# Optimization experiments

Hardware: AMD Instinct MI355X
Metric: run time of the kernel (lower is better)

Reference implementation:

```python
import jax, jax.numpy as jnp
import numpy as np

B, D, A, H, NH = 32768, 768, 17, 128, 4
DH = H // NH


def _ln(x, g, b, eps=1e-5):
    mu = jnp.mean(x, axis=-1, keepdims=True)
    var = jnp.mean((x - mu) ** 2, axis=-1, keepdims=True)
    return (x - mu) / jnp.sqrt(var + eps) * g + b


def setup_inputs() -> dict:
    key = jax.random.key(0)
    ks = jax.random.split(key, 16)
    s = 0.02
    return {
        "visual_feat": jax.random.normal(ks[0], (B, D), jnp.float32),
        "au_feat": jax.random.uniform(ks[1], (B, A), jnp.float32),
        "w_tok": jax.random.normal(ks[2], (H, 1), jnp.float32) * s,
        "b_tok": jnp.zeros((H,), jnp.float32),
        "pos": jax.random.normal(ks[3], (1, A, H), jnp.float32) * s,
        "g_auln": jnp.ones((H,), jnp.float32),
        "b_auln": jnp.zeros((H,), jnp.float32),
        "w_q": jax.random.normal(ks[4], (H, D), jnp.float32) * s,
        "b_q": jnp.zeros((H,), jnp.float32),
        "w_in": jax.random.normal(ks[5], (3 * H, H), jnp.float32) * s,  # packed q,k,v in_proj
        "b_in": jnp.zeros((3 * H,), jnp.float32),
        "w_ao": jax.random.normal(ks[6], (H, H), jnp.float32) * s,  # MHA out_proj
        "b_ao": jnp.zeros((H,), jnp.float32),
        "g_aln": jnp.ones((H,), jnp.float32),
        "b_aln": jnp.zeros((H,), jnp.float32),
        "w_out": jax.random.normal(ks[7], (D, H), jnp.float32) * s,
        "b_out": jnp.zeros((D,), jnp.float32),
        "w_gate": jax.random.normal(ks[8], (D, 2 * D), jnp.float32) * s,
        "b_gate": jnp.zeros((D,), jnp.float32),
    }


def reference(visual_feat, au_feat, w_tok, b_tok, pos, g_auln, b_auln,
              w_q, b_q, w_in, b_in, w_ao, b_ao, g_aln, b_aln,
              w_out, b_out, w_gate, b_gate):
    # AU tokens: Linear(1 -> H) on intensities, + pos embed, LN. [B, A, H]
    au_tokens = au_feat[..., None] * w_tok[:, 0] + b_tok
    au_tokens = _ln(au_tokens + pos, g_auln, b_auln)
    # query: [B, H] (seq len 1)
    query = visual_feat @ w_q.T + b_q
    # MultiheadAttention (batch_first, packed in_proj)
    wq, wk, wv = w_in[:H], w_in[H:2 * H], w_in[2 * H:]
    bq, bk, bv = b_in[:H], b_in[H:2 * H], b_in[2 * H:]
    q = (query @ wq.T + bq).reshape(-1, NH, DH)          # [B, nh, dh]
    k = (au_tokens @ wk.T + bk).reshape(-1, A, NH, DH)   # [B, A, nh, dh]
    v = (au_tokens @ wv.T + bv).reshape(-1, A, NH, DH)
    scale = 1.0 / jnp.sqrt(jnp.asarray(DH, q.dtype))
    scores = jnp.einsum('bhd,bahd->bha', q * scale, k)   # [B, nh, A]
    attn = jax.nn.softmax(scores, axis=-1)
    ctx = jnp.einsum('bha,bahd->bhd', attn, v).reshape(-1, H)
    attn_out = ctx @ w_ao.T + b_ao
    attn_out = _ln(attn_out, g_aln, b_aln)
    attn_feat = attn_out @ w_out.T + b_out               # [B, D]
    gate_in = jnp.concatenate([visual_feat, attn_feat], axis=1)
    gate = jax.nn.sigmoid(gate_in @ w_gate.T + b_gate)
    return gate * attn_feat + (1.0 - gate) * visual_feat
```

## Files before the change

### kernel.cpp

```cpp
#include <hip/hip_runtime.h>
#include <hip/hip_bf16.h>

typedef __hip_bfloat16 bf16;
typedef __attribute__((ext_vector_type(8))) short short8;
typedef __attribute__((ext_vector_type(4))) float f32x4;
typedef __attribute__((ext_vector_type(8))) __bf16 bf16x8;

#define NB 32768
#define DD 768
#define AA 17
#define HH 128

__device__ __forceinline__ float bs2f(short s){
  unsigned int u = ((unsigned int)(unsigned short)s) << 16;
  return __builtin_bit_cast(float, u);
}
__device__ __forceinline__ short f2bs(float f){
  bf16 h = __float2bfloat16(f);
  return __builtin_bit_cast(short, h);
}
__device__ __forceinline__ f32x4 mfma16(short8 a, short8 b, f32x4 c){
  return __builtin_amdgcn_mfma_f32_16x16x32_bf16(
      __builtin_bit_cast(bf16x8, a), __builtin_bit_cast(bf16x8, b), c, 0, 0, 0);
}

template<int F32>
__device__ __forceinline__ short8 ldchunk(const void* base, long elem_off){
  if (F32){
    const float4* p = (const float4*)((const float*)base + elem_off);
    float4 x = p[0], y = p[1];
    short8 r;
    r[0]=f2bs(x.x); r[1]=f2bs(x.y); r[2]=f2bs(x.z); r[3]=f2bs(x.w);
    r[4]=f2bs(y.x); r[5]=f2bs(y.y); r[6]=f2bs(y.z); r[7]=f2bs(y.w);
    return r;
  } else {
    return *(const short8*)((const short*)base + elem_off);
  }
}


__device__ __forceinline__ float blk_mean128(float v, float* tmp){
  int t = threadIdx.x;
  #pragma unroll
  for (int m = 32; m; m >>= 1) v += __shfl_xor(v, m);
  if ((t & 63) == 0) tmp[t >> 6] = v;
  __syncthreads();
  float r = (tmp[0] + tmp[1]) * (1.0f / 128.0f);
  __syncthreads();
  return r;
}

__global__ void prep1(const float* __restrict__ w_tok, const float* __restrict__ b_tok,
                      const float* __restrict__ pos, const float* __restrict__ g_auln,
                      float* __restrict__ ug, float* __restrict__ rg, float* __restrict__ coef){
  __shared__ float tmp[2];
  int h = threadIdx.x;
  float w = w_tok[h];
  float wbar = blk_mean128(w, tmp);
  float u = w - wbar;
  float g = g_auln[h];
  ug[h] = u * g;
  float muu = blk_mean128(u * u, tmp);
  if (h == 0) coef[0] = muu;
  float bt = b_tok[h];
  for (int a = 0; a < AA; ++a){
    float c = bt + pos[a * HH + h];
    float cbar = blk_mean128(c, tmp);
    float r = c - cbar;
    rg[a * HH + h] = r * g;
    float mur = blk_mean128(u * r, tmp);
    float mrr = blk_mean128(r * r, tmp);
    if (h == 0){ coef[1 + a] = mur; coef[18 + a] = mrr; }
  }
}

__global__ void prep2(const float* __restrict__ w_in, const float* __restrict__ b_in,
                      const float* __restrict__ b_auln, const float* __restrict__ b_q,
                      const float* __restrict__ ug, const float* __restrict__ rg,
                      float* __restrict__ Uk, float* __restrict__ Ck,
                      float* __restrict__ Uv, float* __restrict__ Cv,
                      float* __restrict__ Rk, float* __restrict__ Rv,
                      float* __restrict__ bqf){
  int hp = threadIdx.x, bid = blockIdx.x;
  const float* wqrow = w_in + (long)hp * HH;
  const float* wkrow = w_in + (long)(HH + hp) * HH;
  const float* wvrow = w_in + (long)(2 * HH + hp) * HH;
  if (bid < AA){
    int a = bid;
    float sk = 0.f, sv = 0.f;
    for (int t = 0; t < HH; ++t){
      float r = rg[a * HH + t];
      sk += r * wkrow[t];
      sv += r * wvrow[t];
    }
    Rk[a * HH + hp] = sk; Rv[a * HH + hp] = sv;
  } else if (bid == AA){
    float uk = 0.f, uv = 0.f, ck = 0.f, cv = 0.f;
    for (int t = 0; t < HH; ++t){
      float u = ug[t], ba = b_auln[t];
      float wk = wkrow[t], wv = wvrow[t];
      uk += u * wk; uv += u * wv; ck += ba * wk; cv += ba * wv;
    }
    Uk[hp] = uk; Uv[hp] = uv;
    Ck[hp] = ck + b_in[HH + hp];
    Cv[hp] = cv + b_in[2 * HH + hp];
  } else {
    float s = 0.f;
    for (int t = 0; t < HH; ++t) s += b_q[t] * wqrow[t];
    bqf[hp] = s + b_in[hp];
  }
}

__global__ void prep_wqf(const float* __restrict__ w_in, const float* __restrict__ w_q,
                         bf16* __restrict__ Wqf){
  __shared__ float wq[HH];
  int h = blockIdx.x, t = threadIdx.x;
  if (t < HH) wq[t] = w_in[(long)h * HH + t];
  __syncthreads();
  for (int j = t; j < DD; j += 256){
    float acc = 0.f;
    for (int k = 0; k < HH; ++k) acc += wq[k] * w_q[(long)k * DD + j];
    Wqf[(long)h * DD + j] = __float2bfloat16(acc);
  }
}

__global__ __launch_bounds__(128) void attn(
    const bf16* __restrict__ Q, const float* __restrict__ au, const float* __restrict__ coef,
    const float* __restrict__ Uk_, const float* __restrict__ Ck_,
    const float* __restrict__ Uv_, const float* __restrict__ Cv_,
    const float* __restrict__ Rk, const float* __restrict__ Rv,
    bf16* __restrict__ ctx){
  const int ROWS = 8;
  int h = threadIdx.x;
  long row0 = (long)blockIdx.x * ROWS;
  float Uk = Uk_[h], Ck = Ck_[h], Uv = Uv_[h], Cv = Cv_[h];
  float cA = coef[0];
  __shared__ float sa[ROWS * AA];
  for (int idx = h; idx < ROWS * AA; idx += 128)
    sa[idx] = au[row0 * AA + idx];
  __syncthreads();
  const float scale = 0.17677669529663689f;
  for (int r = 0; r < ROWS; ++r){
    long row = row0 + r;
    float q = __bfloat162float(Q[row * HH + h]);
    float sc[AA], vv[AA];
    #pragma unroll
    for (int a = 0; a < AA; ++a){
      float s = sa[r * AA + a];
      float var = fmaf(s * s, cA, fmaf(2.f * s, coef[1 + a], coef[18 + a]));
      float rinv = rsqrtf(fmaxf(var, 0.f) + 1e-5f);
      float kk = fmaf(s, Uk, Rk[a * HH + h]) * rinv + Ck;
      vv[a]    = fmaf(s, Uv, Rv[a * HH + h]) * rinv + Cv;
      float p = q * kk;
      p += __shfl_xor(p, 16); p += __shfl_xor(p, 8); p += __shfl_xor(p, 4);
      p += __shfl_xor(p, 2);  p += __shfl_xor(p, 1);
      sc[a] = p * scale;
    }
    float mx = sc[0];
    #pragma unroll
    for (int a = 1; a < AA; ++a) mx = fmaxf(mx, sc[a]);
    float den = 0.f, cval = 0.f;
    #pragma unroll
    for (int a = 0; a < AA; ++a){
      float e = __expf(sc[a] - mx);
      den += e; cval += e * vv[a];
    }
    ctx[row * HH + h] = __float2bfloat16(cval / den);
  }
}

template<int AF, int BF>
__device__ __forceinline__ void gemm_phase(
    const void* __restrict__ A, long lda, int ks, int ko,
    const void* __restrict__ B, long ldb,
    long rowBase, int colBase,
    short* As, short* Bs, int tid, int w, int fr, int kq,
    f32x4 (&acc)[2][8])
{
  const int sr0 = tid >> 2,         sp0 = (tid & 3) * 8;
  const int sr1 = (tid + 256) >> 2, sp1 = (tid & 3) * 8;
  for (int kt = 0; kt < ks; ++kt){
    const long kA = (long)kt * 32;
    const long kB = ko + kA;
    short8 av0 = ldchunk<AF>(A, (rowBase + sr0) * lda + kA + sp0);
    short8 av1 = ldchunk<AF>(A, (rowBase + sr1) * lda + kA + sp1);
    short8 bv0 = ldchunk<BF>(B, (long)(colBase + sr0) * ldb + kB + sp0);
    short8 bv1 = ldchunk<BF>(B, (long)(colBase + sr1) * ldb + kB + sp1);
    __syncthreads();
    *(short8*)(As + sr0 * 40 + sp0) = av0;
    *(short8*)(As + sr1 * 40 + sp1) = av1;
    *(short8*)(Bs + sr0 * 40 + sp0) = bv0;
    *(short8*)(Bs + sr1 * 40 + sp1) = bv1;
    __syncthreads();
    const int ra0 = w * 32 + fr;
    short8 a0 = *(const short8*)(As + ra0 * 40 + kq * 8);
    short8 a1 = *(const short8*)(As + (ra0 + 16) * 40 + kq * 8);
    #pragma unroll
    for (int nt = 0; nt < 8; ++nt){
      short8 b = *(const short8*)(Bs + (nt * 16 + fr) * 40 + kq * 8);
      acc[0][nt] = mfma16(a0, b, acc[0][nt]);
      acc[1][nt] = mfma16(a1, b, acc[1][nt]);
    }
  }
}

template<int MODE, int A1F, int A2F, int BF>
__global__ __launch_bounds__(256) void gemm_bt(
    const void* __restrict__ A1, long lda1, int k1,
    const void* __restrict__ A2, long lda2, int k2, int koff2,
    const void* __restrict__ Bw, long ldb,
    const float* __restrict__ bias,
    const float* __restrict__ g_ln, const float* __restrict__ b_ln,
    const float* __restrict__ vf, const bf16* __restrict__ af,
    void* __restrict__ C, long ldc)
{
  __shared__ __align__(16) short smem[128 * 136];
  short* As = smem;
  short* Bs = smem + 5120;
  const int tid = threadIdx.x;
  const int w = tid >> 6, l = tid & 63;
  const long rowBase = (long)blockIdx.y * 128;
  const int colBase = blockIdx.x * 128;
  const int fr = l & 15;
  const int kq = l >> 4;

  f32x4 acc[2][8];
  f32x4 zero = {0.f, 0.f, 0.f, 0.f};
  #pragma unroll
  for (int i = 0; i < 2; ++i)
    #pragma unroll
    for (int j = 0; j < 8; ++j) acc[i][j] = zero;

  gemm_phase<A1F, BF>(A1, lda1, k1, 0, Bw, ldb, rowBase, colBase, As, Bs, tid, w, fr, kq, acc);
  if (MODE == 3)
    gemm_phase<A2F, BF>(A2, lda2, k2, koff2, Bw, ldb, rowBase, colBase, As, Bs, tid, w, fr, kq, acc);
  __syncthreads();

  short* ep = smem;
  if (MODE == 1){
    #pragma unroll
    for (int mt = 0; mt < 2; ++mt){
      #pragma unroll
      for (int r = 0; r < 4; ++r){
        float x[8]; float sm = 0.f, sq = 0.f;
        #pragma unroll
        for (int nt = 0; nt < 8; ++nt){
          const int col = colBase + nt * 16 + fr;
          x[nt] = acc[mt][nt][r] + bias[col];
          sm += x[nt]; sq += x[nt] * x[nt];
        }
        sm += __shfl_xor(sm, 1); sq += __shfl_xor(sq, 1);
        sm += __shfl_xor(sm, 2); sq += __shfl_xor(sq, 2);
        sm += __shfl_xor(sm, 4); sq += __shfl_xor(sq, 4);
        sm += __shfl_xor(sm, 8); sq += __shfl_xor(sq, 8);
        const float mu = sm * (1.f / 128.f);
        const float var = sq * (1.f / 128.f) - mu * mu;
        const float rinv = rsqrtf(fmaxf(var, 0.f) + 1e-5f);
        const int lrow = w * 32 + mt * 16 + kq * 4 + r;
        #pragma unroll
        for (int nt = 0; nt < 8; ++nt){
          const int col = colBase + nt * 16 + fr;
          float y = (x[nt] - mu) * rinv * g_ln[col] + b_ln[col];
          ep[lrow * 136 + nt * 16 + fr] = f2bs(y);
        }
      }
    }
  } else {
    #pragma unroll
    for (int nt = 0; nt < 8; ++nt){
      const int col = colBase + nt * 16 + fr;
      const float bv = bias[col];
      #pragma unroll
      for (int mt = 0; mt < 2; ++mt){
        const int lrow0 = w * 32 + mt * 16 + kq * 4;
        #pragma unroll
        for (int r = 0; r < 4; ++r)
          ep[(lrow0 + r) * 136 + nt * 16 + fr] = f2bs(acc[mt][nt][r] + bv);
      }
    }
  }
  __syncthreads();

  #pragma unroll
  for (int it = 0; it < 8; ++it){
    const int cid = tid + it * 256;
    const int rw = cid >> 4;
    const int cc = (cid & 15) * 8;
    const long gr = rowBase + rw;
    short8 vls = *(const short8*)(ep + rw * 136 + cc);
    if (MODE == 3){
      const float4* vp = (const float4*)(vf + gr * ldc + colBase + cc);
      const float4 v0 = vp[0], v1 = vp[1];
      const float vv[8] = {v0.x, v0.y, v0.z, v0.w, v1.x, v1.y, v1.z, v1.w};
      const short8 afv = *(const short8*)((const short*)af + gr * ldc + colBase + cc);
      float o[8];
      #pragma unroll
      for (int e = 0; e < 8; ++e){
        const float lin = bs2f(vls[e]);
        const float gate = 1.f / (1.f + __expf(-lin));
        o[e] = gate * bs2f(afv[e]) + (1.f - gate) * vv[e];
      }
      float* cp = (float*)C + gr * ldc + colBase + cc;
      *(float4*)cp       = {o[0], o[1], o[2], o[3]};
      *(float4*)(cp + 4) = {o[4], o[5], o[6], o[7]};
    } else {
      short* cp = (short*)C + gr * ldc + colBase + cc;
      *(short8*)cp = vls;
    }
  }
}

extern "C" void kernel_launch(void* const* d_in, const int* in_sizes, int n_in,
                              void* d_out, int out_size, void* d_ws, size_t ws_size,
                              hipStream_t stream){
  const float* visual = (const float*)d_in[0];
  const float* au     = (const float*)d_in[1];
  const float* w_tok  = (const float*)d_in[2];
  const float* b_tok  = (const float*)d_in[3];
  const float* pos    = (const float*)d_in[4];
  const float* g_auln = (const float*)d_in[5];
  const float* b_auln = (const float*)d_in[6];
  const float* w_q    = (const float*)d_in[7];
  const float* b_q    = (const float*)d_in[8];
  const float* w_in   = (const float*)d_in[9];
  const float* b_in   = (const float*)d_in[10];
  const float* w_ao   = (const float*)d_in[11];
  const float* b_ao   = (const float*)d_in[12];
  const float* g_aln  = (const float*)d_in[13];
  const float* b_aln  = (const float*)d_in[14];
  const float* w_out  = (const float*)d_in[15];
  const float* b_out  = (const float*)d_in[16];
  const float* w_gate = (const float*)d_in[17];
  const float* b_gate = (const float*)d_in[18];

  char* ob = (char*)d_out;
  bf16* Q   = (bf16*)(ob);
  bf16* ctx = (bf16*)(ob + ((size_t)8 << 20));
  bf16* aon = (bf16*)(ob + ((size_t)16 << 20));
  char* p = ob + ((size_t)24 << 20);
  auto alloc = [&](size_t bytes){ char* r = p; p += (bytes + 255) & ~(size_t)255; return r; };
  bf16*  Wqf  = (bf16*) alloc((size_t)HH * DD * 2);
  float* bqf  = (float*)alloc(HH * 4);
  float* ug   = (float*)alloc(HH * 4);
  float* rg   = (float*)alloc(AA * HH * 4);
  float* coef = (float*)alloc(64 * 4);
  float* Uk   = (float*)alloc(HH * 4);
  float* Ck   = (float*)alloc(HH * 4);
  float* Uv   = (float*)alloc(HH * 4);
  float* Cv   = (float*)alloc(HH * 4);
  float* Rk   = (float*)alloc(AA * HH * 4);
  float* Rv   = (float*)alloc(AA * HH * 4);
  bf16*  af   = (bf16*)d_ws;

  prep1<<<dim3(1), dim3(128), 0, stream>>>(w_tok, b_tok, pos, g_auln, ug, rg, coef);
  prep2<<<dim3(19), dim3(128), 0, stream>>>(w_in, b_in, b_auln, b_q, ug, rg, Uk, Ck, Uv, Cv, Rk, Rv, bqf);
  prep_wqf<<<dim3(128), dim3(256), 0, stream>>>(w_in, w_q, Wqf);

  gemm_bt<0, 1, 0, 0><<<dim3(1, NB / 128), dim3(256), 0, stream>>>(
      visual, (long)DD, DD / 32,
      nullptr, 0L, 0, 0,
      Wqf, (long)DD,
      bqf, nullptr, nullptr, nullptr, nullptr,
      Q, (long)HH);

  attn<<<dim3(NB / 8), dim3(128), 0, stream>>>(Q, au, coef, Uk, Ck, Uv, Cv, Rk, Rv, ctx);

  gemm_bt<1, 0, 0, 1><<<dim3(1, NB / 128), dim3(256), 0, stream>>>(
      ctx, (long)HH, HH / 32,
      nullptr, 0L, 0, 0,
      w_ao, (long)HH,
      b_ao, g_aln, b_aln, nullptr, nullptr,
      aon, (long)HH);

  gemm_bt<2, 0, 0, 1><<<dim3(DD / 128, NB / 128), dim3(256), 0, stream>>>(
      aon, (long)HH, HH / 32,
      nullptr, 0L, 0, 0,
      w_out, (long)HH,
      b_out, nullptr, nullptr, nullptr, nullptr,
      af, (long)DD);

  gemm_bt<3, 1, 0, 1><<<dim3(DD / 128, NB / 128), dim3(256), 0, stream>>>(
      visual, (long)DD, DD / 32,
      af, (long)DD, DD / 32, DD,
      w_gate, (long)(2 * DD),
      b_gate, nullptr, nullptr, visual, af,
      (float*)d_out, (long)DD);
}
```

Before: 555.1 us.

## Fold out-projection into gate GEMM and fuse final gating into one kernel

Precomputes w_gate[:,D:]·w_out and the folded gate bias so the gate logit's second half becomes a K=128 GEMM on the normalized attention output. The attn_feat GEMM is computed in the same kernel, so the bf16 attn_feat intermediate is never written or reread. The Q GEMM also writes a bf16 copy of visual_feat to the workspace, letting the final kernel read half the bytes for its K=768 operand. This adds a per-call weight-prep kernel and a small precision change from folding the weights in bf16. The final epilogue now uses scalar strided stores.

```diff
diff --git a/kernel.cpp b/kernel.cpp
--- a/kernel.cpp
+++ b/kernel.cpp
@@ -124,6 +124,32 @@
   }
 }
 
+__global__ void prep_gate(const float* __restrict__ w_gate, const float* __restrict__ b_gate,
+                          const float* __restrict__ w_out, const float* __restrict__ b_out,
+                          bf16* __restrict__ Wg1b, bf16* __restrict__ Wg2w,
+                          bf16* __restrict__ Woutb, float* __restrict__ bgp){
+  __shared__ float wg2[DD];
+  __shared__ float red[2];
+  int c = blockIdx.x, t = threadIdx.x;
+  const float* wrow = w_gate + (long)c * (2 * DD);
+  for (int j = t; j < DD; j += 128){
+    Wg1b[(long)c * DD + j] = __float2bfloat16(wrow[j]);
+    wg2[j] = wrow[DD + j];
+  }
+  __syncthreads();
+  float acc = 0.f;
+  for (int j = 0; j < DD; ++j) acc = fmaf(wg2[j], w_out[(long)j * HH + t], acc);
+  Wg2w[(long)c * HH + t] = __float2bfloat16(acc);
+  Woutb[(long)c * HH + t] = __float2bfloat16(w_out[(long)c * HH + t]);
+  float pb = 0.f;
+  for (int j = t; j < DD; j += 128) pb = fmaf(wg2[j], b_out[j], pb);
+  #pragma unroll
+  for (int m = 32; m; m >>= 1) pb += __shfl_xor(pb, m);
+  if ((t & 63) == 0) red[t >> 6] = pb;
+  __syncthreads();
+  if (t == 0) bgp[c] = b_gate[c] + red[0] + red[1];
+}
+
 __global__ __launch_bounds__(128) void attn(
     const bf16* __restrict__ Q, const float* __restrict__ au, const float* __restrict__ coef,
     const float* __restrict__ Uk_, const float* __restrict__ Ck_,
@@ -169,50 +195,14 @@
   }
 }
 
-template<int AF, int BF>
-__device__ __forceinline__ void gemm_phase(
-    const void* __restrict__ A, long lda, int ks, int ko,
-    const void* __restrict__ B, long ldb,
-    long rowBase, int colBase,
-    short* As, short* Bs, int tid, int w, int fr, int kq,
-    f32x4 (&acc)[2][8])
-{
-  const int sr0 = tid >> 2,         sp0 = (tid & 3) * 8;
-  const int sr1 = (tid + 256) >> 2, sp1 = (tid & 3) * 8;
-  for (int kt = 0; kt < ks; ++kt){
-    const long kA = (long)kt * 32;
-    const long kB = ko + kA;
-    short8 av0 = ldchunk<AF>(A, (rowBase + sr0) * lda + kA + sp0);
-    short8 av1 = ldchunk<AF>(A, (rowBase + sr1) * lda + kA + sp1);
-    short8 bv0 = ldchunk<BF>(B, (long)(colBase + sr0) * ldb + kB + sp0);
-    short8 bv1 = ldchunk<BF>(B, (long)(colBase + sr1) * ldb + kB + sp1);
-    __syncthreads();
-    *(short8*)(As + sr0 * 40 + sp0) = av0;
-    *(short8*)(As + sr1 * 40 + sp1) = av1;
-    *(short8*)(Bs + sr0 * 40 + sp0) = bv0;
-    *(short8*)(Bs + sr1 * 40 + sp1) = bv1;
-    __syncthreads();
-    const int ra0 = w * 32 + fr;
-    short8 a0 = *(const short8*)(As + ra0 * 40 + kq * 8);
-    short8 a1 = *(const short8*)(As + (ra0 + 16) * 40 + kq * 8);
-    #pragma unroll
-    for (int nt = 0; nt < 8; ++nt){
-      short8 b = *(const short8*)(Bs + (nt * 16 + fr) * 40 + kq * 8);
-      acc[0][nt] = mfma16(a0, b, acc[0][nt]);
-      acc[1][nt] = mfma16(a1, b, acc[1][nt]);
-    }
-  }
-}
-
-template<int MODE, int A1F, int A2F, int BF>
+template<int MODE, int AF, int BF, int SIDE>
 __global__ __launch_bounds__(256) void gemm_bt(
-    const void* __restrict__ A1, long lda1, int k1,
-    const void* __restrict__ A2, long lda2, int k2, int koff2,
+    const void* __restrict__ A, long lda, int ks,
     const void* __restrict__ Bw, long ldb,
     const float* __restrict__ bias,
     const float* __restrict__ g_ln, const float* __restrict__ b_ln,
-    const float* __restrict__ vf, const bf16* __restrict__ af,
-    void* __restrict__ C, long ldc)
+    short* __restrict__ sideA,
+    bf16* __restrict__ C, long ldc)
 {
   __shared__ __align__(16) short smem[128 * 136];
   short* As = smem;
@@ -223,6 +213,8 @@
   const int colBase = blockIdx.x * 128;
   const int fr = l & 15;
   const int kq = l >> 4;
+  const int sr0 = tid >> 2,         sp0 = (tid & 3) * 8;
+  const int sr1 = (tid + 256) >> 2;
 
   f32x4 acc[2][8];
   f32x4 zero = {0.f, 0.f, 0.f, 0.f};
@@ -231,9 +223,32 @@
     #pragma unroll
     for (int j = 0; j < 8; ++j) acc[i][j] = zero;
 
-  gemm_phase<A1F, BF>(A1, lda1, k1, 0, Bw, ldb, rowBase, colBase, As, Bs, tid, w, fr, kq, acc);
-  if (MODE == 3)
-    gemm_phase<A2F, BF>(A2, lda2, k2, koff2, Bw, ldb, rowBase, colBase, As, Bs, tid, w, fr, kq, acc);
+  for (int kt = 0; kt < ks; ++kt){
+    const long kA = (long)kt * 32;
+    short8 av0 = ldchunk<AF>(A, (rowBase + sr0) * lda + kA + sp0);
+    short8 av1 = ldchunk<AF>(A, (rowBase + sr1) * lda + kA + sp0);
+    short8 bv0 = ldchunk<BF>(Bw, (long)(colBase + sr0) * ldb + kA + sp0);
+    short8 bv1 = ldchunk<BF>(Bw, (long)(colBase + sr1) * ldb + kA + sp0);
+    if (SIDE){
+      *(short8*)(sideA + (rowBase + sr0) * lda + kA + sp0) = av0;
+      *(short8*)(sideA + (rowBase + sr1) * lda + kA + sp0) = av1;
+    }
+    __syncthreads();
+    *(short8*)(As + sr0 * 40 + sp0) = av0;
+    *(short8*)(As + sr1 * 40 + sp0) = av1;
+    *(short8*)(Bs + sr0 * 40 + sp0) = bv0;
+    *(short8*)(Bs + sr1 * 40 + sp0) = bv1;
+    __syncthreads();
+    const int ra0 = w * 32 + fr;
+    short8 a0 = *(const short8*)(As + ra0 * 40 + kq * 8);
+    short8 a1 = *(const short8*)(As + (ra0 + 16) * 40 + kq * 8);
+    #pragma unroll
+    for (int nt = 0; nt < 8; ++nt){
+      short8 b = *(const short8*)(Bs + (nt * 16 + fr) * 40 + kq * 8);
+      acc[0][nt] = mfma16(a0, b, acc[0][nt]);
+      acc[1][nt] = mfma16(a1, b, acc[1][nt]);
+    }
+  }
   __syncthreads();
 
   short* ep = smem;
@@ -288,24 +303,118 @@
     const int cc = (cid & 15) * 8;
     const long gr = rowBase + rw;
     short8 vls = *(const short8*)(ep + rw * 136 + cc);
-    if (MODE == 3){
-      const float4* vp = (const float4*)(vf + gr * ldc + colBase + cc);
-      const float4 v0 = vp[0], v1 = vp[1];
-      const float vv[8] = {v0.x, v0.y, v0.z, v0.w, v1.x, v1.y, v1.z, v1.w};
-      const short8 afv = *(const short8*)((const short*)af + gr * ldc + colBase + cc);
-      float o[8];
+    short* cp = (short*)C + gr * ldc + colBase + cc;
+    *(short8*)cp = vls;
+  }
+}
+
+template<int A1F>
+__global__ __launch_bounds__(256) void gemm_final(
+    const void* __restrict__ A1,
+    const bf16* __restrict__ aon,
+    const bf16* __restrict__ Wg1b,
+    const bf16* __restrict__ Wg2w,
+    const bf16* __restrict__ Woutb,
+    const float* __restrict__ bgp,
+    const float* __restrict__ b_out,
+    const float* __restrict__ vf,
+    float* __restrict__ C)
+{
+  __shared__ __align__(16) short As[128 * 40];
+  __shared__ __align__(16) short Bs[128 * 40];
+  __shared__ __align__(16) short Bs2[128 * 40];
+  const int tid = threadIdx.x;
+  const int w = tid >> 6, l = tid & 63;
+  const long rowBase = (long)blockIdx.y * 128;
+  const int colBase = blockIdx.x * 128;
+  const int fr = l & 15;
+  const int kq = l >> 4;
+  const int sr0 = tid >> 2,         sp0 = (tid & 3) * 8;
+  const int sr1 = (tid + 256) >> 2;
+
+  f32x4 accG[2][8], accF[2][8];
+  f32x4 zero = {0.f, 0.f, 0.f, 0.f};
+  #pragma unroll
+  for (int i = 0; i < 2; ++i)
+    #pragma unroll
+    for (int j = 0; j < 8; ++j){ accG[i][j] = zero; accF[i][j] = zero; }
+
+  for (int kt = 0; kt < DD / 32; ++kt){
+    const long kA = (long)kt * 32;
+    short8 av0 = ldchunk<A1F>(A1, (rowBase + sr0) * DD + kA + sp0);
+    short8 av1 = ldchunk<A1F>(A1, (rowBase + sr1) * DD + kA + sp0);
+    short8 bv0 = *(const short8*)((const short*)Wg1b + (long)(colBase + sr0) * DD + kA + sp0);
+    short8 bv1 = *(const short8*)((const short*)Wg1b + (long)(colBase + sr1) * DD + kA + sp0);
+    __syncthreads();
+    *(short8*)(As + sr0 * 40 + sp0) = av0;
+    *(short8*)(As + sr1 * 40 + sp0) = av1;
+    *(short8*)(Bs + sr0 * 40 + sp0) = bv0;
+    *(short8*)(Bs + sr1 * 40 + sp0) = bv1;
+    __syncthreads();
+    const int ra0 = w * 32 + fr;
+    short8 a0 = *(const short8*)(As + ra0 * 40 + kq * 8);
+    short8 a1 = *(const short8*)(As + (ra0 + 16) * 40 + kq * 8);
+    #pragma unroll
+    for (int nt = 0; nt < 8; ++nt){
+      short8 b = *(const short8*)(Bs + (nt * 16 + fr) * 40 + kq * 8);
+      accG[0][nt] = mfma16(a0, b, accG[0][nt]);
+      accG[1][nt] = mfma16(a1, b, accG[1][nt]);
+    }
+  }
+
+  for (int kt = 0; kt < HH / 32; ++kt){
+    const long kA = (long)kt * 32;
+    short8 av0 = *(const short8*)((const short*)aon + (rowBase + sr0) * HH + kA + sp0);
+    short8 av1 = *(const short8*)((const short*)aon + (rowBase + sr1) * HH + kA + sp0);
+    short8 bv0 = *(const short8*)((const short*)Wg2w + (long)(colBase + sr0) * HH + kA + sp0);
+    short8 bv1 = *(const short8*)((const short*)Wg2w + (long)(colBase + sr1) * HH + kA + sp0);
+    short8 cv0 = *(const short8*)((const short*)Woutb + (long)(colBase + sr0) * HH + kA + sp0);
+    short8 cv1 = *(const short8*)((const short*)Woutb + (long)(colBase + sr1) * HH + kA + sp0);
+    __syncthreads();
+    *(short8*)(As + sr0 * 40 + sp0) = av0;
+    *(short8*)(As + sr1 * 40 + sp0) = av1;
+    *(short8*)(Bs + sr0 * 40 + sp0) = bv0;
+    *(short8*)(Bs + sr1 * 40 + sp0) = bv1;
+    *(short8*)(Bs2 + sr0 * 40 + sp0) = cv0;
+    *(short8*)(Bs2 + sr1 * 40 + sp0) = cv1;
+    __syncthreads();
+    const int ra0 = w * 32 + fr;
+    short8 a0 = *(const short8*)(As + ra0 * 40 + kq * 8);
+    short8 a1 = *(const short8*)(As + (ra0 + 16) * 40 + kq * 8);
+    #pragma unroll
+    for (int nt = 0; nt < 8; ++nt){
+      short8 b  = *(const short8*)(Bs  + (nt * 16 + fr) * 40 + kq * 8);
+      short8 b2 = *(const short8*)(Bs2 + (nt * 16 + fr) * 40 + kq * 8);
+      accG[0][nt] = mfma16(a0, b,  accG[0][nt]);
+      accG[1][nt] = mfma16(a1, b,  accG[1][nt]);
+      accF[0][nt] = mfma16(a0, b2, accF[0][nt]);
+      accF[1][nt] = mfma16(a1, b2, accF[1][nt]);
+    }
+  }
+
+  float bg[8], bo[8];
+  #pragma unroll
+  for (int nt = 0; nt < 8; ++nt){
+    const int col = colBase + nt * 16 + fr;
+    bg[nt] = bgp[col];
+    bo[nt] = b_out[col];
+  }
+  #pragma unroll
+  for (int mt = 0; mt < 2; ++mt){
+    const long r0 = rowBase + w * 32 + mt * 16 + kq * 4;
+    #pragma unroll
+    for (int r = 0; r < 4; ++r){
+      const long row = r0 + r;
+      const float* vrow = vf + row * DD;
+      float* crow = C + row * DD;
       #pragma unroll
-      for (int e = 0; e < 8; ++e){
-        const float lin = bs2f(vls[e]);
+      for (int nt = 0; nt < 8; ++nt){
+        const int col = colBase + nt * 16 + fr;
+        const float lin = accG[mt][nt][r] + bg[nt];
+        const float afv = accF[mt][nt][r] + bo[nt];
         const float gate = 1.f / (1.f + __expf(-lin));
-        o[e] = gate * bs2f(afv[e]) + (1.f - gate) * vv[e];
+        crow[col] = gate * afv + (1.f - gate) * vrow[col];
       }
-      float* cp = (float*)C + gr * ldc + colBase + cc;
-      *(float4*)cp       = {o[0], o[1], o[2], o[3]};
-      *(float4*)(cp + 4) = {o[4], o[5], o[6], o[7]};
-    } else {
-      short* cp = (short*)C + gr * ldc + colBase + cc;
-      *(short8*)cp = vls;
     }
   }
 }
@@ -336,8 +445,7 @@
   char* ob = (char*)d_out;
   bf16* Q   = (bf16*)(ob);
   bf16* ctx = (bf16*)(ob + ((size_t)8 << 20));
-  bf16* aon = (bf16*)(ob + ((size_t)16 << 20));
-  char* p = ob + ((size_t)24 << 20);
+  char* p = ob + ((size_t)16 << 20);
   auto alloc = [&](size_t bytes){ char* r = p; p += (bytes + 255) & ~(size_t)255; return r; };
   bf16*  Wqf  = (bf16*) alloc((size_t)HH * DD * 2);
   float* bqf  = (float*)alloc(HH * 4);
@@ -350,39 +458,41 @@
   float* Cv   = (float*)alloc(HH * 4);
   float* Rk   = (float*)alloc(AA * HH * 4);
   float* Rv   = (float*)alloc(AA * HH * 4);
-  bf16*  af   = (bf16*)d_ws;
+
+  char* q = (char*)d_ws;
+  auto walloc = [&](size_t bytes){ char* r = q; q += (bytes + 255) & ~(size_t)255; return r; };
+  bf16*  aon   = (bf16*) walloc((size_t)NB * HH * 2);
+  bf16*  Wg1b  = (bf16*) walloc((size_t)DD * DD * 2);
+  bf16*  Wg2w  = (bf16*) walloc((size_t)DD * HH * 2);
+  bf16*  Woutb = (bf16*) walloc((size_t)DD * HH * 2);
+  float* bgp   = (float*)walloc(DD * 4);
+  bf16*  vbf   = (bf16*) walloc((size_t)NB * DD * 2);
+  const bool use_vbf = (size_t)(q - (char*)d_ws) <= ws_size;
 
   prep1<<<dim3(1), dim3(128), 0, stream>>>(w_tok, b_tok, pos, g_auln, ug, rg, coef);
   prep2<<<dim3(19), dim3(128), 0, stream>>>(w_in, b_in, b_auln, b_q, ug, rg, Uk, Ck, Uv, Cv, Rk, Rv, bqf);
   prep_wqf<<<dim3(128), dim3(256), 0, stream>>>(w_in, w_q, Wqf);
-
-  gemm_bt<0, 1, 0, 0><<<dim3(1, NB / 128), dim3(256), 0, stream>>>(
-      visual, (long)DD, DD / 32,
-      nullptr, 0L, 0, 0,
-      Wqf, (long)DD,
-      bqf, nullptr, nullptr, nullptr, nullptr,
-      Q, (long)HH);
+  prep_gate<<<dim3(DD), dim3(128), 0, stream>>>(w_gate, b_gate, w_out, b_out, Wg1b, Wg2w, Woutb, bgp);
+
+  if (use_vbf)
+    gemm_bt<0, 1, 0, 1><<<dim3(1, NB / 128), dim3(256), 0, stream>>>(
+        visual, (long)DD, DD / 32, Wqf, (long)DD,
+        bqf, nullptr, nullptr, (short*)vbf, Q, (long)HH);
+  else
+    gemm_bt<0, 1, 0, 0><<<dim3(1, NB / 128), dim3(256), 0, stream>>>(
+        visual, (long)DD, DD / 32, Wqf, (long)DD,
+        bqf, nullptr, nullptr, nullptr, Q, (long)HH);
 
   attn<<<dim3(NB / 8), dim3(128), 0, stream>>>(Q, au, coef, Uk, Ck, Uv, Cv, Rk, Rv, ctx);
 
-  gemm_bt<1, 0, 0, 1><<<dim3(1, NB / 128), dim3(256), 0, stream>>>(
-      ctx, (long)HH, HH / 32,
-      nullptr, 0L, 0, 0,
-      w_ao, (long)HH,
-      b_ao, g_aln, b_aln, nullptr, nullptr,
-      aon, (long)HH);
-
-  gemm_bt<2, 0, 0, 1><<<dim3(DD / 128, NB / 128), dim3(256), 0, stream>>>(
-      aon, (long)HH, HH / 32,
-      nullptr, 0L, 0, 0,
-      w_out, (long)HH,
-      b_out, nullptr, nullptr, nullptr, nullptr,
-      af, (long)DD);
-
-  gemm_bt<3, 1, 0, 1><<<dim3(DD / 128, NB / 128), dim3(256), 0, stream>>>(
-      visual, (long)DD, DD / 32,
-      af, (long)DD, DD / 32, DD,
-      w_gate, (long)(2 * DD),
-      b_gate, nullptr, nullptr, visual, af,
-      (float*)d_out, (long)DD);
-}
+  gemm_bt<1, 0, 1, 0><<<dim3(1, NB / 128), dim3(256), 0, stream>>>(
+      ctx, (long)HH, HH / 32, w_ao, (long)HH,
+      b_ao, g_aln, b_aln, nullptr, aon, (long)HH);
+
+  if (use_vbf)
+    gemm_final<0><<<dim3(DD / 128, NB / 128), dim3(256), 0, stream>>>(
+        vbf, aon, Wg1b, Wg2w, Woutb, bgp, b_out, visual, (float*)d_out);
+  else
+    gemm_final<1><<<dim3(DD / 128, NB / 128), dim3(256), 0, stream>>>(
+        visual, aon, Wg1b, Wg2w, Woutb, bgp, b_out, visual, (float*)d_out);
+}
```

New measurement: 532.7 us. 1.04x faster.
